# Kernel optimization log

Hardware: AMD Instinct MI355X
Metric: run time of the kernel (lower is better)

The kernel has to match this reference:

```python
import jax, jax.numpy as jnp
import numpy as np

D = 1024
L_COMP = 16384
L_FULL = 32768
EPS = 1e-4


def setup_inputs() -> dict:
    key = jax.random.key(0)
    k1, k2 = jax.random.split(key)
    x = jax.random.normal(k1, (1, L_COMP, D), dtype=jnp.float32)
    p_selected = jax.random.uniform(k2, (L_COMP,), dtype=jnp.float32)
    # boundary mask over full sequence: exactly L_COMP ones, first position forced to 1
    rng = np.random.default_rng(0)
    pos = np.concatenate([[0], np.sort(rng.choice(np.arange(1, L_FULL), L_COMP - 1, replace=False))])
    b_np = np.zeros((1, L_FULL), dtype=np.int32)
    b_np[0, pos] = 1
    b = jnp.asarray(b_np)
    return {"x": x, "p_selected": p_selected, "b": b}


def _ema_scan(x, p):
    # z_t = (1 - p_t) * z_{t-1} + p_t * x_t  (exact math of the mamba chunk scan
    # with A=-1, dt=log(1/(1-p)), B=p, C=1, x pre-divided by dt)
    a = jnp.broadcast_to((1.0 - p)[None, :, None], x.shape)  # (1, L, d) decay
    bxt = p[None, :, None] * x                                # (1, L, d) input term

    def combine(c1, c2):
        a1, b1 = c1
        a2, b2 = c2
        return a1 * a2, a2 * b1 + b2

    _, z = jax.lax.associative_scan(combine, (a, bxt), axis=1)
    return z


def reference(x, p_selected, b):
    p = jnp.clip(p_selected.astype(jnp.float32), EPS, 1.0 - EPS)  # (L_comp,)
    z_bar = _ema_scan(x.astype(jnp.float32), p)                   # (1, L_comp, d)
    plug_back_idx = jnp.cumsum(b, axis=1) - 1                     # (1, L_full)
    out = jnp.take(z_bar[0], plug_back_idx[0], axis=0)[None]      # (1, L_full, d)
    return out.astype(x.dtype)
```

## Files before the change

### kernel.cpp

```cpp
#include <hip/hip_runtime.h>


#define DCH 1024
#define L_COMP 16384
#define L_FULL 32768
#define CHUNK 32
#define NCHUNK (L_COMP / CHUNK)
#define SEG (L_FULL / NCHUNK)
#define EPSV 1e-4f

typedef float v4f __attribute__((ext_vector_type(4)));

__device__ __forceinline__ float clipp(float p) {
    p = fmaxf(p, EPSV);
    return fminf(p, 1.0f - EPSV);
}

__global__ __launch_bounds__(256, 2) void chunk_kernel(
    const float* __restrict__ x, const float* __restrict__ p,
    const int* __restrict__ b,
    float* __restrict__ Bbuf, float* __restrict__ Abuf, int* __restrict__ bsum) {
    const int c = blockIdx.x;
    const int tid = threadIdx.x;
    const int lane = tid & 63;
    const int wave = tid >> 6;
    const int base = c * CHUNK;

    const v4f* x4 = reinterpret_cast<const v4f*>(x) + (size_t)base * (DCH / 4) + tid;
    v4f h = (v4f)0.f;
    float aprod = 1.0f;
    for (int ib = 0; ib < CHUNK; ib += 8) {
        v4f xv[8];
        float pv[8];
#pragma unroll
        for (int j = 0; j < 8; ++j) {
            xv[j] = x4[(ib + j) * (DCH / 4)];
            pv[j] = clipp(p[base + ib + j]);
        }
#pragma unroll
        for (int j = 0; j < 8; ++j) {
            float a = 1.0f - pv[j];
            h = a * h + pv[j] * xv[j];
            aprod *= a;
        }
    }
    reinterpret_cast<v4f*>(Bbuf)[c * (DCH / 4) + tid] = h;
    if (tid == 0) Abuf[c] = aprod;
    if (wave == 0) {
        int v = b[c * SEG + lane];
        int s = v;
#pragma unroll
        for (int off = 1; off < 64; off <<= 1) s += __shfl_xor(s, off, 64);
        if (lane == 0) bsum[c] = s;
    }
}

__global__ __launch_bounds__(256, 2) void dechunk_kernel(
    const float* __restrict__ x, const float* __restrict__ p,
    const int* __restrict__ b, float* __restrict__ out,
    const float* __restrict__ Bbuf, const float* __restrict__ Abuf,
    const int* __restrict__ bsum) {
    const int c = blockIdx.x;
    const int tid = threadIdx.x;
    const int lane = tid & 63;
    const int wave = tid >> 6;
    const int base = c * CHUNK;

    __shared__ int bpref[NCHUNK + 1];
    __shared__ int spos[CHUNK + 1];
    __shared__ int wtot[4];

    {
        int v0 = bsum[2 * tid];
        int v1 = bsum[2 * tid + 1];
        int s = v0 + v1;
        int incl = s;
#pragma unroll
        for (int off = 1; off < 64; off <<= 1) {
            int n = __shfl_up(incl, off, 64);
            if (lane >= off) incl += n;
        }
        if (lane == 63) wtot[wave] = incl;
        __syncthreads();
        int woff = 0;
        for (int w = 0; w < wave; ++w) woff += wtot[w];
        int ex = woff + incl - s;
        bpref[2 * tid] = ex;
        bpref[2 * tid + 1] = ex + v0;
        if (tid == 0) bpref[NCHUNK] = L_COMP;
        __syncthreads();
    }

    if (tid <= CHUNK) {
        int t = base + tid;
        int posv = L_FULL;
        if (t < L_COMP) {
            int lo = 0, hi = NCHUNK;
            while (hi - lo > 1) {
                int mid = (lo + hi) >> 1;
                if (bpref[mid] <= t) lo = mid; else hi = mid;
            }
            int lr = t - bpref[lo];
            const int4* bseg = reinterpret_cast<const int4*>(b) + lo * (SEG / 4);
            int cnt = 0;
#pragma unroll 4
            for (int q = 0; q < SEG / 4; ++q) {
                int4 w = bseg[q];
                if (w.x) { if (cnt == lr) posv = lo * SEG + 4 * q + 0; ++cnt; }
                if (w.y) { if (cnt == lr) posv = lo * SEG + 4 * q + 1; ++cnt; }
                if (w.z) { if (cnt == lr) posv = lo * SEG + 4 * q + 2; ++cnt; }
                if (w.w) { if (cnt == lr) posv = lo * SEG + 4 * q + 3; ++cnt; }
            }
        }
        spos[tid] = posv;
    }

    v4f h = (v4f)0.f;
    {
        const v4f* B4 = reinterpret_cast<const v4f*>(Bbuf) + tid;
        int k = 0;
        for (; k + 16 <= c; k += 16) {
            v4f bv[16];
            float av[16];
#pragma unroll
            for (int j = 0; j < 16; ++j) {
                bv[j] = B4[(k + j) * (DCH / 4)];
                av[j] = Abuf[k + j];
            }
#pragma unroll
            for (int j = 0; j < 16; ++j)
                h = av[j] * h + bv[j];
        }
        for (; k < c; ++k) {
            v4f bv = B4[k * (DCH / 4)];
            h = Abuf[k] * h + bv;
        }
    }
    __syncthreads();

    {
        const v4f* x4 = reinterpret_cast<const v4f*>(x) + (size_t)base * (DCH / 4) + tid;
        v4f* out4 = reinterpret_cast<v4f*>(out) + tid;
        int f0 = spos[0];
        for (int ib = 0; ib < CHUNK; ib += 8) {
            v4f xv[8];
            float pv[8];
            int fe[8];
#pragma unroll
            for (int j = 0; j < 8; ++j) {
                xv[j] = x4[(ib + j) * (DCH / 4)];
                pv[j] = clipp(p[base + ib + j]);
                fe[j] = spos[ib + j + 1];
            }
#pragma unroll
            for (int j = 0; j < 8; ++j) {
                float a = 1.0f - pv[j];
                h = a * h + pv[j] * xv[j];
                for (int f = f0; f < fe[j]; ++f) {
                    __builtin_nontemporal_store(h, &out4[(size_t)f * (DCH / 4)]);
                }
                f0 = fe[j];
            }
        }
    }
}

extern "C" void kernel_launch(void* const* d_in, const int* in_sizes, int n_in,
                              void* d_out, int out_size, void* d_ws, size_t ws_size,
                              hipStream_t stream) {
    const float* x = (const float*)d_in[0];
    const float* p = (const float*)d_in[1];
    const int* b = (const int*)d_in[2];
    float* out = (float*)d_out;

    char* ws = (char*)d_ws;
    float* Abuf = (float*)ws;
    int* bsum = (int*)(ws + 4096);
    float* Bbuf = (float*)(ws + 8192);

    chunk_kernel<<<NCHUNK, 256, 0, stream>>>(x, p, b, Bbuf, Abuf, bsum);
    dechunk_kernel<<<NCHUNK, 256, 0, stream>>>(x, p, b, out, Bbuf, Abuf, bsum);
}
```

Before: 211.9 us.

## Fuse chunk and dechunk kernels into single-pass decoupled look-back scan

Merges the two kernels into one launch in which each block takes a dynamic ticket, computes its chunk summary while keeping x in registers, publishes it with a release flag, then walks back over predecessors' summaries. The walk-back stops once the accumulated decay weight falls below a tiny threshold. Each block also recomputes the boundary-count prefix directly from b instead of reading per-chunk sums. This removes the second pass over x, one launch, and the full O(c) prefix loop per block. In exchange it relies on spin-waiting on other blocks' flags, truncates the prefix approximately, adds a memset launch, and makes every block reread the whole b mask.

```diff
diff --git a/kernel.cpp b/kernel.cpp
--- a/kernel.cpp
+++ b/kernel.cpp
@@ -8,6 +8,7 @@
 #define NCHUNK (L_COMP / CHUNK)
 #define SEG (L_FULL / NCHUNK)
 #define EPSV 1e-4f
+#define WMIN 1e-12f
 
 typedef float v4f __attribute__((ext_vector_type(4)));
 
@@ -16,63 +17,64 @@
     return fminf(p, 1.0f - EPSV);
 }
 
-__global__ __launch_bounds__(256, 2) void chunk_kernel(
+__global__ __launch_bounds__(256, 2) void fused_kernel(
     const float* __restrict__ x, const float* __restrict__ p,
-    const int* __restrict__ b,
-    float* __restrict__ Bbuf, float* __restrict__ Abuf, int* __restrict__ bsum) {
-    const int c = blockIdx.x;
+    const int* __restrict__ b, float* __restrict__ out,
+    float* __restrict__ Bbuf, float* __restrict__ Apub,
+    int* __restrict__ flag, int* __restrict__ ticket) {
     const int tid = threadIdx.x;
     const int lane = tid & 63;
     const int wave = tid >> 6;
-    const int base = c * CHUNK;
-
-    const v4f* x4 = reinterpret_cast<const v4f*>(x) + (size_t)base * (DCH / 4) + tid;
-    v4f h = (v4f)0.f;
-    float aprod = 1.0f;
-    for (int ib = 0; ib < CHUNK; ib += 8) {
-        v4f xv[8];
-        float pv[8];
-#pragma unroll
-        for (int j = 0; j < 8; ++j) {
-            xv[j] = x4[(ib + j) * (DCH / 4)];
-            pv[j] = clipp(p[base + ib + j]);
-        }
-#pragma unroll
-        for (int j = 0; j < 8; ++j) {
-            float a = 1.0f - pv[j];
-            h = a * h + pv[j] * xv[j];
-            aprod *= a;
-        }
-    }
-    reinterpret_cast<v4f*>(Bbuf)[c * (DCH / 4) + tid] = h;
-    if (tid == 0) Abuf[c] = aprod;
-    if (wave == 0) {
-        int v = b[c * SEG + lane];
-        int s = v;
-#pragma unroll
-        for (int off = 1; off < 64; off <<= 1) s += __shfl_xor(s, off, 64);
-        if (lane == 0) bsum[c] = s;
-    }
-}
-
-__global__ __launch_bounds__(256, 2) void dechunk_kernel(
-    const float* __restrict__ x, const float* __restrict__ p,
-    const int* __restrict__ b, float* __restrict__ out,
-    const float* __restrict__ Bbuf, const float* __restrict__ Abuf,
-    const int* __restrict__ bsum) {
-    const int c = blockIdx.x;
-    const int tid = threadIdx.x;
-    const int lane = tid & 63;
-    const int wave = tid >> 6;
-    const int base = c * CHUNK;
 
     __shared__ int bpref[NCHUNK + 1];
     __shared__ int spos[CHUNK + 1];
     __shared__ int wtot[4];
+    __shared__ int vcs;
+
+    if (tid == 0) vcs = atomicAdd(ticket, 1);
+    __syncthreads();
+    const int c = vcs;
+    const int base = c * CHUNK;
+
+    v4f xv[CHUNK];
+    v4f h = (v4f)0.f;
+    float aprod = 1.0f;
+    {
+        const v4f* x4 = reinterpret_cast<const v4f*>(x) + (size_t)base * (DCH / 4) + tid;
+#pragma unroll
+        for (int ib = 0; ib < CHUNK; ib += 8) {
+            float pvv[8];
+#pragma unroll
+            for (int j = 0; j < 8; ++j) {
+                xv[ib + j] = x4[(ib + j) * (DCH / 4)];
+                pvv[j] = clipp(p[base + ib + j]);
+            }
+#pragma unroll
+            for (int j = 0; j < 8; ++j) {
+                float a = 1.0f - pvv[j];
+                h = a * h + pvv[j] * xv[ib + j];
+                aprod *= a;
+            }
+        }
+    }
+    reinterpret_cast<v4f*>(Bbuf)[c * (DCH / 4) + tid] = h;
+    if (tid == 0) Apub[c] = aprod;
+    __syncthreads();
+    if (tid == 0) {
+        __threadfence();
+        __hip_atomic_store(&flag[c], 1, __ATOMIC_RELEASE, __HIP_MEMORY_SCOPE_AGENT);
+    }
 
     {
-        int v0 = bsum[2 * tid];
-        int v1 = bsum[2 * tid + 1];
+        const int4* b4 = reinterpret_cast<const int4*>(b);
+        int v0 = 0, v1 = 0;
+#pragma unroll 4
+        for (int q = 0; q < SEG / 4; ++q) {
+            int4 w0 = b4[(2 * tid) * (SEG / 4) + q];
+            int4 w1 = b4[(2 * tid + 1) * (SEG / 4) + q];
+            v0 += w0.x + w0.y + w0.z + w0.w;
+            v1 += w1.x + w1.y + w1.z + w1.w;
+        }
         int s = v0 + v1;
         int incl = s;
 #pragma unroll
@@ -114,53 +116,37 @@
         }
         spos[tid] = posv;
     }
+    __syncthreads();
 
-    v4f h = (v4f)0.f;
+    v4f hpre = (v4f)0.f;
     {
+        float w = 1.0f;
         const v4f* B4 = reinterpret_cast<const v4f*>(Bbuf) + tid;
-        int k = 0;
-        for (; k + 16 <= c; k += 16) {
-            v4f bv[16];
-            float av[16];
-#pragma unroll
-            for (int j = 0; j < 16; ++j) {
-                bv[j] = B4[(k + j) * (DCH / 4)];
-                av[j] = Abuf[k + j];
-            }
-#pragma unroll
-            for (int j = 0; j < 16; ++j)
-                h = av[j] * h + bv[j];
-        }
-        for (; k < c; ++k) {
-            v4f bv = B4[k * (DCH / 4)];
-            h = Abuf[k] * h + bv;
+        for (int k = c - 1; k >= 0; --k) {
+            if (w < WMIN) break;
+            while (__hip_atomic_load(&flag[k], __ATOMIC_ACQUIRE,
+                                     __HIP_MEMORY_SCOPE_AGENT) == 0)
+                __builtin_amdgcn_s_sleep(1);
+            v4f bk = B4[k * (DCH / 4)];
+            float ak = Apub[k];
+            hpre += w * bk;
+            w *= ak;
         }
     }
-    __syncthreads();
 
     {
-        const v4f* x4 = reinterpret_cast<const v4f*>(x) + (size_t)base * (DCH / 4) + tid;
+        v4f hh = hpre;
         v4f* out4 = reinterpret_cast<v4f*>(out) + tid;
         int f0 = spos[0];
-        for (int ib = 0; ib < CHUNK; ib += 8) {
-            v4f xv[8];
-            float pv[8];
-            int fe[8];
 #pragma unroll
-            for (int j = 0; j < 8; ++j) {
-                xv[j] = x4[(ib + j) * (DCH / 4)];
-                pv[j] = clipp(p[base + ib + j]);
-                fe[j] = spos[ib + j + 1];
-            }
-#pragma unroll
-            for (int j = 0; j < 8; ++j) {
-                float a = 1.0f - pv[j];
-                h = a * h + pv[j] * xv[j];
-                for (int f = f0; f < fe[j]; ++f) {
-                    __builtin_nontemporal_store(h, &out4[(size_t)f * (DCH / 4)]);
-                }
-                f0 = fe[j];
-            }
+        for (int t = 0; t < CHUNK; ++t) {
+            float pt = clipp(p[base + t]);
+            float a = 1.0f - pt;
+            hh = a * hh + pt * xv[t];
+            int fe = spos[t + 1];
+            for (int f = f0; f < fe; ++f)
+                __builtin_nontemporal_store(hh, &out4[(size_t)f * (DCH / 4)]);
+            f0 = fe;
         }
     }
 }
@@ -174,10 +160,11 @@
     float* out = (float*)d_out;
 
     char* ws = (char*)d_ws;
-    float* Abuf = (float*)ws;
-    int* bsum = (int*)(ws + 4096);
+    float* Apub = (float*)ws;
+    int* flag = (int*)(ws + 4096);
+    int* ticket = (int*)(ws + 6144);
     float* Bbuf = (float*)(ws + 8192);
 
-    chunk_kernel<<<NCHUNK, 256, 0, stream>>>(x, p, b, Bbuf, Abuf, bsum);
-    dechunk_kernel<<<NCHUNK, 256, 0, stream>>>(x, p, b, out, Bbuf, Abuf, bsum);
+    hipMemsetAsync(ws + 4096, 0, 4096, stream);
+    fused_kernel<<<NCHUNK, 256, 0, stream>>>(x, p, b, out, Bbuf, Apub, flag, ticket);
 }
```

Measured after the change: 244.7 us. +15.5%, slower.

## Fuse chunk and dechunk kernels with truncated local lookback recompute

Applied to the files above, without the earlier changes.

Drops the separate chunk-summary kernel and the O(c) sequential carry-in over all previous chunk states. Each block now walks back over preceding chunks only until the accumulated decay product falls below 1e-12, then recomputes the carry-in state directly from x and p. Each block also recomputes the per-segment boundary counts from b instead of reading precomputed sums. This removes a launch and the quadratic-in-chunks state traffic. In exchange it adds redundant reads of b per block and a tiny truncation error, and blocks scan much further back when p values are small.

```diff
diff --git a/kernel.cpp b/kernel.cpp
--- a/kernel.cpp
+++ b/kernel.cpp
@@ -8,6 +8,7 @@
 #define NCHUNK (L_COMP / CHUNK)
 #define SEG (L_FULL / NCHUNK)
 #define EPSV 1e-4f
+#define WMIN 1e-12f
 
 typedef float v4f __attribute__((ext_vector_type(4)));
 
@@ -16,50 +17,9 @@
     return fminf(p, 1.0f - EPSV);
 }
 
-__global__ __launch_bounds__(256, 2) void chunk_kernel(
+__global__ __launch_bounds__(256, 2) void fused_kernel(
     const float* __restrict__ x, const float* __restrict__ p,
-    const int* __restrict__ b,
-    float* __restrict__ Bbuf, float* __restrict__ Abuf, int* __restrict__ bsum) {
-    const int c = blockIdx.x;
-    const int tid = threadIdx.x;
-    const int lane = tid & 63;
-    const int wave = tid >> 6;
-    const int base = c * CHUNK;
-
-    const v4f* x4 = reinterpret_cast<const v4f*>(x) + (size_t)base * (DCH / 4) + tid;
-    v4f h = (v4f)0.f;
-    float aprod = 1.0f;
-    for (int ib = 0; ib < CHUNK; ib += 8) {
-        v4f xv[8];
-        float pv[8];
-#pragma unroll
-        for (int j = 0; j < 8; ++j) {
-            xv[j] = x4[(ib + j) * (DCH / 4)];
-            pv[j] = clipp(p[base + ib + j]);
-        }
-#pragma unroll
-        for (int j = 0; j < 8; ++j) {
-            float a = 1.0f - pv[j];
-            h = a * h + pv[j] * xv[j];
-            aprod *= a;
-        }
-    }
-    reinterpret_cast<v4f*>(Bbuf)[c * (DCH / 4) + tid] = h;
-    if (tid == 0) Abuf[c] = aprod;
-    if (wave == 0) {
-        int v = b[c * SEG + lane];
-        int s = v;
-#pragma unroll
-        for (int off = 1; off < 64; off <<= 1) s += __shfl_xor(s, off, 64);
-        if (lane == 0) bsum[c] = s;
-    }
-}
-
-__global__ __launch_bounds__(256, 2) void dechunk_kernel(
-    const float* __restrict__ x, const float* __restrict__ p,
-    const int* __restrict__ b, float* __restrict__ out,
-    const float* __restrict__ Bbuf, const float* __restrict__ Abuf,
-    const int* __restrict__ bsum) {
+    const int* __restrict__ b, float* __restrict__ out) {
     const int c = blockIdx.x;
     const int tid = threadIdx.x;
     const int lane = tid & 63;
@@ -71,8 +31,15 @@
     __shared__ int wtot[4];
 
     {
-        int v0 = bsum[2 * tid];
-        int v1 = bsum[2 * tid + 1];
+        const int4* b4 = reinterpret_cast<const int4*>(b);
+        int v0 = 0, v1 = 0;
+#pragma unroll 4
+        for (int q = 0; q < SEG / 4; ++q) {
+            int4 w0 = b4[(2 * tid) * (SEG / 4) + q];
+            int4 w1 = b4[(2 * tid + 1) * (SEG / 4) + q];
+            v0 += w0.x + w0.y + w0.z + w0.w;
+            v1 += w1.x + w1.y + w1.z + w1.w;
+        }
         int s = v0 + v1;
         int incl = s;
 #pragma unroll
@@ -114,32 +81,38 @@
         }
         spos[tid] = posv;
     }
+    __syncthreads();
 
-    v4f h = (v4f)0.f;
+    int kstart = c;
     {
-        const v4f* B4 = reinterpret_cast<const v4f*>(Bbuf) + tid;
-        int k = 0;
-        for (; k + 16 <= c; k += 16) {
-            v4f bv[16];
-            float av[16];
+        float w = 1.0f;
+        while (kstart > 0 && w >= WMIN) {
+            --kstart;
+            float ap = 1.0f;
+#pragma unroll 8
+            for (int t = 0; t < CHUNK; ++t)
+                ap *= (1.0f - clipp(p[kstart * CHUNK + t]));
+            w *= ap;
+        }
+    }
+
+    {
+        const v4f* x4 = reinterpret_cast<const v4f*>(x) + tid;
+        v4f h = (v4f)0.f;
+        for (int r = kstart * CHUNK; r < base; r += 8) {
+            v4f xv[8];
+            float pv[8];
 #pragma unroll
-            for (int j = 0; j < 16; ++j) {
-                bv[j] = B4[(k + j) * (DCH / 4)];
-                av[j] = Abuf[k + j];
+            for (int j = 0; j < 8; ++j) {
+                xv[j] = x4[(size_t)(r + j) * (DCH / 4)];
+                pv[j] = clipp(p[r + j]);
             }
 #pragma unroll
-            for (int j = 0; j < 16; ++j)
-                h = av[j] * h + bv[j];
+            for (int j = 0; j < 8; ++j) {
+                float a = 1.0f - pv[j];
+                h = a * h + pv[j] * xv[j];
+            }
         }
-        for (; k < c; ++k) {
-            v4f bv = B4[k * (DCH / 4)];
-            h = Abuf[k] * h + bv;
-        }
-    }
-    __syncthreads();
-
-    {
-        const v4f* x4 = reinterpret_cast<const v4f*>(x) + (size_t)base * (DCH / 4) + tid;
         v4f* out4 = reinterpret_cast<v4f*>(out) + tid;
         int f0 = spos[0];
         for (int ib = 0; ib < CHUNK; ib += 8) {
@@ -148,7 +121,7 @@
             int fe[8];
 #pragma unroll
             for (int j = 0; j < 8; ++j) {
-                xv[j] = x4[(ib + j) * (DCH / 4)];
+                xv[j] = x4[(size_t)(base + ib + j) * (DCH / 4)];
                 pv[j] = clipp(p[base + ib + j]);
                 fe[j] = spos[ib + j + 1];
             }
@@ -172,12 +145,7 @@
     const float* p = (const float*)d_in[1];
     const int* b = (const int*)d_in[2];
     float* out = (float*)d_out;
+    (void)d_ws; (void)ws_size;
 
-    char* ws = (char*)d_ws;
-    float* Abuf = (float*)ws;
-    int* bsum = (int*)(ws + 4096);
-    float* Bbuf = (float*)(ws + 8192);
-
-    chunk_kernel<<<NCHUNK, 256, 0, stream>>>(x, p, b, Bbuf, Abuf, bsum);
-    dechunk_kernel<<<NCHUNK, 256, 0, stream>>>(x, p, b, out, Bbuf, Abuf, bsum);
+    fused_kernel<<<NCHUNK, 256, 0, stream>>>(x, p, b, out);
 }
```

Result: faster. 204.2 us (-3.6%).
